# Performance work log

Measured on AMD Instinct MI355X. Metric: run time of the kernel, lower is better.

## Reference

```python
import jax, jax.numpy as jnp
import numpy as np

D_MODEL = 1024
NHEAD = 16
HEAD_DIM = D_MODEL // NHEAD
WINDOW = 64


def setup_inputs() -> dict:
    key = jax.random.key(0)
    ks = jax.random.split(key, 5)
    B, S = 1, 4096
    x = jax.random.normal(ks[0], (B, S, D_MODEL), dtype=jnp.float32)
    scale = 0.02
    Wq = jax.random.normal(ks[1], (D_MODEL, D_MODEL), dtype=jnp.float32) * scale
    Wk = jax.random.normal(ks[2], (D_MODEL, D_MODEL), dtype=jnp.float32) * scale
    Wv = jax.random.normal(ks[3], (D_MODEL, D_MODEL), dtype=jnp.float32) * scale
    Wo = jax.random.normal(ks[4], (D_MODEL, D_MODEL), dtype=jnp.float32) * scale
    return {"x": x, "Wq": Wq, "Wk": Wk, "Wv": Wv, "Wo": Wo}


def reference(x, Wq, Wk, Wv, Wo):
    B, S, D = x.shape
    H, hd, W = NHEAD, HEAD_DIM, WINDOW
    # projections (torch Linear: y = x @ W.T)
    q = (x @ Wq.T).reshape(B, S, H, hd).transpose(0, 2, 1, 3)  # [B,H,S,hd]
    k = (x @ Wk.T).reshape(B, S, H, hd).transpose(0, 2, 1, 3)
    v = (x @ Wv.T).reshape(B, S, H, hd).transpose(0, 2, 1, 3)
    # sliding window indices: each query attends to [i-W+1, i]
    qpos = jnp.arange(S)
    offsets = jnp.arange(-W + 1, 1)
    key_idx = qpos[:, None] + offsets[None, :]          # [S,W]
    valid = (key_idx >= 0) & (key_idx < S)
    key_idx = jnp.clip(key_idx, 0, S - 1)
    # gather windows: [B,H,S,W,hd]
    kw = jnp.take(k, key_idx, axis=2)
    vw = jnp.take(v, key_idx, axis=2)
    scores = jnp.einsum('bhsd,bhswd->bhsw', q, kw) / (hd ** 0.5)
    scores = jnp.where(valid[None, None, :, :], scores, -jnp.inf)
    attn = jax.nn.softmax(scores, axis=-1)
    out = jnp.einsum('bhsw,bhswd->bhsd', attn, vw)      # [B,H,S,hd]
    out = out.transpose(0, 2, 1, 3).reshape(B, S, D)
    return out @ Wo.T
```

## Files before the change

kernel.cpp:

```cpp
#include <hip/hip_runtime.h>
#include <cstdint>

typedef unsigned short u16;
using bf16x8 = __attribute__((ext_vector_type(8))) short;
using u16x8  = __attribute__((ext_vector_type(8))) unsigned short;
using f32x4  = __attribute__((ext_vector_type(4))) float;

#define DM 1024

__device__ __forceinline__ u16 f2b(float f) {
    union { float f; unsigned u; } v; v.f = f;
    unsigned r = v.u + 0x7FFFu + ((v.u >> 16) & 1u);
    return (u16)(r >> 16);
}
__device__ __forceinline__ float b2f(u16 b) {
    union { unsigned u; float f; } v; v.u = ((unsigned)b) << 16;
    return v.f;
}

#define GLL(gp, lp) __builtin_amdgcn_global_load_lds( \
    (const __attribute__((address_space(1))) void*)(uintptr_t)(gp), \
    (__attribute__((address_space(3))) void*)(unsigned)(uintptr_t)(lp), 16, 0, 0)

#define BAR()    __builtin_amdgcn_s_barrier()
#define WAITV4() asm volatile("s_waitcnt vmcnt(4)" ::: "memory")
#define WAITV0() asm volatile("s_waitcnt vmcnt(0)" ::: "memory")

__global__ __launch_bounds__(256) void cvt_all(const float* __restrict__ x,
                                               const float* __restrict__ Wq,
                                               const float* __restrict__ Wk,
                                               const float* __restrict__ Wv,
                                               const float* __restrict__ Wo,
                                               u16* __restrict__ xb,
                                               u16* __restrict__ wqkv,
                                               u16* __restrict__ wob) {
    size_t v = ((size_t)blockIdx.x * 256 + threadIdx.x) << 3;
    const float* src; u16* dst; size_t off;
    if (v < (size_t)4194304) { src = x; dst = xb; off = v; }
    else {
        size_t w = v - 4194304; int s = (int)(w >> 20); off = w & 1048575;
        src = (s == 0) ? Wq : (s == 1) ? Wk : (s == 2) ? Wv : Wo;
        dst = (s < 3) ? (wqkv + ((size_t)s << 20)) : wob;
    }
    const f32x4* p = (const f32x4*)(src + off);
    f32x4 a = p[0], b = p[1];
    u16x8 o;
    o[0] = f2b(a[0]); o[1] = f2b(a[1]); o[2] = f2b(a[2]); o[3] = f2b(a[3]);
    o[4] = f2b(b[0]); o[5] = f2b(b[1]); o[6] = f2b(b[2]); o[7] = f2b(b[3]);
    *(u16x8*)(dst + off) = o;
}

#define MROW(af_, bf_, d) \
    acc[d][0] = __builtin_amdgcn_mfma_f32_16x16x32_bf16(af_, bf_[0], acc[d][0], 0, 0, 0); \
    acc[d][1] = __builtin_amdgcn_mfma_f32_16x16x32_bf16(af_, bf_[1], acc[d][1], 0, 0, 0); \
    acc[d][2] = __builtin_amdgcn_mfma_f32_16x16x32_bf16(af_, bf_[2], acc[d][2], 0, 0, 0); \
    acc[d][3] = __builtin_amdgcn_mfma_f32_16x16x32_bf16(af_, bf_[3], acc[d][3], 0, 0, 0);

#define MFMA16(af_, bf_, ib) do { \
    __builtin_amdgcn_s_setprio(1); \
    MROW(af_[0], bf_, (ib) + 0) \
    MROW(af_[1], bf_, (ib) + 1) \
    MROW(af_[2], bf_, (ib) + 2) \
    MROW(af_[3], bf_, (ib) + 3) \
    __builtin_amdgcn_s_setprio(0); } while (0)

__global__ __launch_bounds__(512, 2) void gemm_qkv8(const u16* __restrict__ A,
                                                    const u16* __restrict__ B,
                                                    u16* __restrict__ Q,
                                                    u16* __restrict__ Ko,
                                                    u16* __restrict__ V) {
    __shared__ __align__(16) u16 As[2 * 16384];
    __shared__ __align__(16) u16 Bs[2 * 16384];
    const int tid  = threadIdx.x;
    const int lane = tid & 63;
    const int wid  = tid >> 6;
    const int wr   = wid >> 2;
    const int wc   = wid & 3;
    const int fr   = lane & 15;
    const int fg   = lane >> 4;
    const int brow = blockIdx.y << 8;
    const int bcol = blockIdx.x << 8;

    const int srow = tid >> 3;
    const int scol = ((tid & 7) ^ (srow & 7)) << 3;
    const u16* Ag = A + (size_t)(brow + srow) * 1024 + scol;
    const u16* Bg = B + (size_t)(bcol + srow) * 1024 + scol;

#define STG_A(buf, kt, c) GLL(Ag + (size_t)(c) * 65536 + (kt) * 64, \
                              (char*)As + (buf) * 32768 + (c) * 8192 + (wid << 10))
#define STG_B(buf, kt, c) GLL(Bg + (size_t)(c) * 65536 + (kt) * 64, \
                              (char*)Bs + (buf) * 32768 + (c) * 8192 + (wid << 10))

    const int swz  = (fr & 7) << 3;
    const int col0 = (fg << 3) ^ swz;
    const int col1 = (32 + (fg << 3)) ^ swz;
    const int aro  = ((wr << 7) + fr) << 6;
    const int bro  = ((wc << 6) + fr) << 6;

#define LDA4(dst, bufo, ih, cl) do { \
    const u16* p_ = As + (bufo) + aro + ((ih) << 12) + (cl); \
    dst[0] = *(const bf16x8*)(p_); \
    dst[1] = *(const bf16x8*)(p_ + 1024); \
    dst[2] = *(const bf16x8*)(p_ + 2048); \
    dst[3] = *(const bf16x8*)(p_ + 3072); } while (0)

#define LDB4(dst, bufo, cl) do { \
    const u16* p_ = Bs + (bufo) + bro + (cl); \
    dst[0] = *(const bf16x8*)(p_); \
    dst[1] = *(const bf16x8*)(p_ + 1024); \
    dst[2] = *(const bf16x8*)(p_ + 2048); \
    dst[3] = *(const bf16x8*)(p_ + 3072); } while (0)

    f32x4 acc[8][4];
    const f32x4 z = {0.f, 0.f, 0.f, 0.f};
    #pragma unroll
    for (int i = 0; i < 8; ++i)
        #pragma unroll
        for (int j = 0; j < 4; ++j) acc[i][j] = z;

    bf16x8 af0[4], af1[4], bf0[4], bf1[4];

    STG_B(0, 0, 0); STG_B(0, 0, 1); STG_B(0, 0, 2); STG_B(0, 0, 3);
    STG_A(0, 0, 0); STG_A(0, 0, 1); STG_A(0, 0, 2); STG_A(0, 0, 3);
    STG_B(1, 1, 0); STG_B(1, 1, 1); STG_B(1, 1, 2); STG_B(1, 1, 3);
    WAITV4();
    BAR();

    #pragma unroll 1
    for (int t = 0; t < 7; ++t) {
        const int k1 = 2 * t + 1, k2 = 2 * t + 2, k3 = 2 * t + 3;
        LDA4(af0, 0, 0, col0); LDB4(bf0, 0, col0);
        STG_A(1, k1, 0); STG_A(1, k1, 1);
        BAR(); MFMA16(af0, bf0, 0); BAR();
        LDA4(af1, 0, 0, col1); LDB4(bf1, 0, col1);
        STG_A(1, k1, 2); STG_A(1, k1, 3);
        BAR(); MFMA16(af1, bf1, 0); BAR();
        LDA4(af0, 0, 1, col0);
        STG_B(0, k2, 0); STG_B(0, k2, 1);
        BAR(); MFMA16(af0, bf0, 4); BAR();
        LDA4(af1, 0, 1, col1);
        STG_B(0, k2, 2); STG_B(0, k2, 3);
        BAR(); MFMA16(af1, bf1, 4); WAITV4(); BAR();
        LDA4(af0, 16384, 0, col0); LDB4(bf0, 16384, col0);
        STG_A(0, k2, 0); STG_A(0, k2, 1);
        BAR(); MFMA16(af0, bf0, 0); BAR();
        LDA4(af1, 16384, 0, col1); LDB4(bf1, 16384, col1);
        STG_A(0, k2, 2); STG_A(0, k2, 3);
        BAR(); MFMA16(af1, bf1, 0); BAR();
        LDA4(af0, 16384, 1, col0);
        STG_B(1, k3, 0); STG_B(1, k3, 1);
        BAR(); MFMA16(af0, bf0, 4); BAR();
        LDA4(af1, 16384, 1, col1);
        STG_B(1, k3, 2); STG_B(1, k3, 3);
        BAR(); MFMA16(af1, bf1, 4); WAITV4(); BAR();
    }
    LDA4(af0, 0, 0, col0); LDB4(bf0, 0, col0);
    STG_A(1, 15, 0); STG_A(1, 15, 1);
    BAR(); MFMA16(af0, bf0, 0); BAR();
    LDA4(af1, 0, 0, col1); LDB4(bf1, 0, col1);
    STG_A(1, 15, 2); STG_A(1, 15, 3);
    BAR(); MFMA16(af1, bf1, 0); BAR();
    LDA4(af0, 0, 1, col0);
    BAR(); MFMA16(af0, bf0, 4); BAR();
    LDA4(af1, 0, 1, col1);
    BAR(); MFMA16(af1, bf1, 4); WAITV0(); BAR();
    LDA4(af0, 16384, 0, col0); LDB4(bf0, 16384, col0);
    BAR(); MFMA16(af0, bf0, 0); BAR();
    LDA4(af1, 16384, 0, col1); LDB4(bf1, 16384, col1);
    BAR(); MFMA16(af1, bf1, 0); BAR();
    LDA4(af0, 16384, 1, col0);
    BAR(); MFMA16(af0, bf0, 4); BAR();
    LDA4(af1, 16384, 1, col1);
    BAR(); MFMA16(af1, bf1, 4);

    const int which = bcol >> 10;
    u16* O = (which == 0) ? Q : ((which == 1) ? Ko : V);
    const int ocol0 = (bcol & 1023) + (wc << 6);
    const int orow0 = brow + (wr << 7);
    #pragma unroll
    for (int i = 0; i < 8; ++i)
        #pragma unroll
        for (int j = 0; j < 4; ++j)
            #pragma unroll
            for (int r = 0; r < 4; ++r) {
                const int row = orow0 + i * 16 + fg * 4 + r;
                const int col = ocol0 + j * 16 + fr;
                O[(size_t)row * 1024 + col] = f2b(acc[i][j][r]);
            }
#undef STG_A
#undef STG_B
#undef LDA4
#undef LDB4
}

__device__ __forceinline__ void gemm_core_1024(const u16* __restrict__ A,
                                               const u16* __restrict__ B,
                                               int brow, int bcol,
                                               u16* Asb, u16* Bsb,
                                               f32x4 acc[4][4]) {
    const int tid  = threadIdx.x;
    const int lane = tid & 63;
    const int wid  = tid >> 6;
    const int wrow = (wid >> 1) << 6;
    const int wcol = (wid & 1) << 6;
    const int fr   = lane & 15;
    const int fk   = (lane >> 4) << 3;

    const size_t aBase = (size_t)(brow + (tid >> 2)) * 1024 + ((tid & 3) << 3);
    const size_t bBase = (size_t)(bcol + (tid >> 2)) * 1024 + ((tid & 3) << 3);
    const int wOff = wid << 10;

    const f32x4 z = {0.f, 0.f, 0.f, 0.f};
    #pragma unroll
    for (int i = 0; i < 4; ++i)
        #pragma unroll
        for (int j = 0; j < 4; ++j) acc[i][j] = z;

#define STAGE(bufi, kt) do { \
        const u16* ga_ = A + aBase + ((size_t)(kt) << 5); \
        const u16* gb_ = B + bBase + ((size_t)(kt) << 5); \
        char* la_ = (char*)(Asb + ((bufi) << 12)) + wOff; \
        char* lb_ = (char*)(Bsb + ((bufi) << 12)) + wOff; \
        GLL(ga_, la_); GLL(ga_ + (size_t)64 * 1024, la_ + 4096); \
        GLL(gb_, lb_); GLL(gb_ + (size_t)64 * 1024, lb_ + 4096); \
    } while (0)

    STAGE(0, 0);
    #pragma unroll 2
    for (int kt = 0; kt < 32; ++kt) {
        const int buf = kt & 1;
        __syncthreads();
        if (kt + 1 < 32) STAGE(buf ^ 1, kt + 1);
        const u16* As = Asb + (buf << 12);
        const u16* Bs = Bsb + (buf << 12);
        bf16x8 af[4], bfr[4];
        #pragma unroll
        for (int i = 0; i < 4; ++i)
            af[i] = *(const bf16x8*)(As + ((wrow + (i << 4) + fr) << 5) + fk);
        #pragma unroll
        for (int j = 0; j < 4; ++j)
            bfr[j] = *(const bf16x8*)(Bs + ((wcol + (j << 4) + fr) << 5) + fk);
        #pragma unroll
        for (int i = 0; i < 4; ++i)
            #pragma unroll
            for (int j = 0; j < 4; ++j)
                acc[i][j] = __builtin_amdgcn_mfma_f32_16x16x32_bf16(af[i], bfr[j], acc[i][j], 0, 0, 0);
    }
#undef STAGE
}

__global__ __launch_bounds__(256) void gemm_out(const u16* __restrict__ A,
                                                const u16* __restrict__ B,
                                                float* __restrict__ C) {
    __shared__ __align__(16) u16 As[2 * 128 * 32];
    __shared__ __align__(16) u16 Bs[2 * 128 * 32];
    const int brow = blockIdx.y << 7;
    const int bcol = blockIdx.x << 7;
    f32x4 acc[4][4];
    gemm_core_1024(A, B, brow, bcol, As, Bs, acc);

    const int lane = threadIdx.x & 63;
    const int wid  = threadIdx.x >> 6;
    const int wrow = (wid >> 1) << 6;
    const int wcol = (wid & 1) << 6;
    const int g = lane >> 4, c = lane & 15;
    #pragma unroll
    for (int i = 0; i < 4; ++i)
        #pragma unroll
        for (int j = 0; j < 4; ++j)
            #pragma unroll
            for (int r = 0; r < 4; ++r) {
                const int row = brow + wrow + i * 16 + g * 4 + r;
                const int col = bcol + wcol + j * 16 + c;
                C[(size_t)row * 1024 + col] = acc[i][j][r];
            }
}

__global__ __launch_bounds__(256) void attn_kernel(const u16* __restrict__ Qg,
                                                   const u16* __restrict__ Kg,
                                                   const u16* __restrict__ Vg,
                                                   u16* __restrict__ Og) {
    const int qb  = blockIdx.x;
    const int h   = blockIdx.y;
    const int tid = threadIdx.x;
    const int lane = tid & 63;
    const int w  = tid >> 6;
    const int fr = lane & 15;
    const int fg = lane >> 4;

    __shared__ __align__(16) u16 QK[64 * 72 + 128 * 72];
    __shared__ __align__(16) u16 Vt[64 * 136];
    __shared__ float Mrow[64][4];
    __shared__ float Lrow[64][4];

    u16* Qs = QK;
    u16* Ks = QK + 64 * 72;
    u16* Ps = QK;

    const int hoff  = h * 64;
    const int qrow0 = qb * 64;
    const int krow0 = qrow0 - 64;

    {
        const int r  = tid >> 3;
        const int c0 = (tid & 7) * 8;
        #pragma unroll
        for (int it = 0; it < 2; ++it) {
            const int row = r + it * 32;
            u16x8 val = *(const u16x8*)(Qg + (size_t)(qrow0 + row) * DM + hoff + c0);
            u16x8 o;
            #pragma unroll
            for (int e = 0; e < 8; ++e) o[e] = f2b(b2f(val[e]) * 0.125f);
            *(u16x8*)(Qs + row * 72 + c0) = o;
        }
        #pragma unroll
        for (int it = 0; it < 4; ++it) {
            const int row  = r + it * 32;
            const int grow = krow0 + row;
            u16x8 val = {0, 0, 0, 0, 0, 0, 0, 0};
            if (grow >= 0) val = *(const u16x8*)(Kg + (size_t)grow * DM + hoff + c0);
            *(u16x8*)(Ks + row * 72 + c0) = val;
        }
        #pragma unroll
        for (int it = 0; it < 4; ++it) {
            const int j    = r + it * 32;
            const int grow = krow0 + j;
            u16x8 val = {0, 0, 0, 0, 0, 0, 0, 0};
            if (grow >= 0) val = *(const u16x8*)(Vg + (size_t)grow * DM + hoff + c0);
            #pragma unroll
            for (int e = 0; e < 8; ++e) Vt[(c0 + e) * 136 + j] = val[e];
        }
    }
    __syncthreads();

    const f32x4 z = {0.f, 0.f, 0.f, 0.f};
    f32x4 s[4][2];
    #pragma unroll
    for (int i = 0; i < 4; ++i) { s[i][0] = z; s[i][1] = z; }
    #pragma unroll
    for (int kk = 0; kk < 2; ++kk) {
        const int k0 = kk * 32 + fg * 8;
        bf16x8 aq[4];
        #pragma unroll
        for (int i = 0; i < 4; ++i)
            aq[i] = *(const bf16x8*)(Qs + (i * 16 + fr) * 72 + k0);
        #pragma unroll
        for (int n = 0; n < 2; ++n) {
            const bf16x8 bk = *(const bf16x8*)(Ks + (w * 32 + n * 16 + fr) * 72 + k0);
            #pragma unroll
            for (int i = 0; i < 4; ++i)
                s[i][n] = __builtin_amdgcn_mfma_f32_16x16x32_bf16(aq[i], bk, s[i][n], 0, 0, 0);
        }
    }

    #pragma unroll
    for (int i = 0; i < 4; ++i) {
        #pragma unroll
        for (int r = 0; r < 4; ++r) {
            const int irow = i * 16 + fg * 4 + r;
            float mx = -3.0e38f;
            #pragma unroll
            for (int n = 0; n < 2; ++n) {
                const int jcol = w * 32 + n * 16 + fr;
                const bool valid = (jcol >= irow + 1) && (jcol <= irow + 64) && (krow0 + jcol >= 0);
                const float v = valid ? s[i][n][r] : -3.0e38f;
                s[i][n][r] = v;
                mx = fmaxf(mx, v);
            }
            #pragma unroll
            for (int d = 1; d < 16; d <<= 1) mx = fmaxf(mx, __shfl_xor(mx, d));
            if (fr == 0) Mrow[irow][w] = mx;
        }
    }
    __syncthreads();

    #pragma unroll
    for (int i = 0; i < 4; ++i) {
        #pragma unroll
        for (int r = 0; r < 4; ++r) {
            const int irow = i * 16 + fg * 4 + r;
            const float M = fmaxf(fmaxf(Mrow[irow][0], Mrow[irow][1]),
                                  fmaxf(Mrow[irow][2], Mrow[irow][3]));
            float sum = 0.f;
            #pragma unroll
            for (int n = 0; n < 2; ++n) {
                const float v = s[i][n][r];
                const float p = (v > -1.0e38f) ? __expf(v - M) : 0.f;
                sum += p;
                Ps[irow * 136 + (w * 32 + n * 16 + fr)] = f2b(p);
            }
            #pragma unroll
            for (int d = 1; d < 16; d <<= 1) sum += __shfl_xor(sum, d);
            if (fr == 0) Lrow[irow][w] = sum;
        }
    }
    __syncthreads();

    f32x4 o[4] = {z, z, z, z};
    #pragma unroll
    for (int ks = 0; ks < 4; ++ks) {
        const int k0 = ks * 32 + fg * 8;
        const bf16x8 ap = *(const bf16x8*)(Ps + (w * 16 + fr) * 136 + k0);
        #pragma unroll
        for (int n = 0; n < 4; ++n) {
            const bf16x8 bv = *(const bf16x8*)(Vt + (n * 16 + fr) * 136 + k0);
            o[n] = __builtin_amdgcn_mfma_f32_16x16x32_bf16(ap, bv, o[n], 0, 0, 0);
        }
    }

    #pragma unroll
    for (int r = 0; r < 4; ++r) {
        const int irow = w * 16 + fg * 4 + r;
        const float L = Lrow[irow][0] + Lrow[irow][1] + Lrow[irow][2] + Lrow[irow][3];
        const float rl = 1.0f / L;
        #pragma unroll
        for (int n = 0; n < 4; ++n)
            Og[(size_t)(qrow0 + irow) * DM + hoff + n * 16 + fr] = f2b(o[n][r] * rl);
    }
}

extern "C" void kernel_launch(void* const* d_in, const int* in_sizes, int n_in,
                              void* d_out, int out_size, void* d_ws, size_t ws_size,
                              hipStream_t stream) {
    (void)in_sizes; (void)n_in; (void)out_size; (void)ws_size;
    const float* x  = (const float*)d_in[0];
    const float* Wq = (const float*)d_in[1];
    const float* Wk = (const float*)d_in[2];
    const float* Wv = (const float*)d_in[3];
    const float* Wo = (const float*)d_in[4];
    float* out = (float*)d_out;

    char* ws = (char*)d_ws;
    u16* xb   = (u16*)(ws);
    u16* Wqkv = (u16*)(ws + ((size_t)8  << 20));
    u16* Wob  = (u16*)(ws + ((size_t)14 << 20));
    u16* qb   = (u16*)(ws + ((size_t)16 << 20));
    u16* kb   = (u16*)(ws + ((size_t)24 << 20));
    u16* vb   = (u16*)(ws + ((size_t)32 << 20));
    u16* ab   = (u16*)(ws + ((size_t)40 << 20));

    cvt_all<<<4096, 256, 0, stream>>>(x, Wq, Wk, Wv, Wo, xb, Wqkv, Wob);
    gemm_qkv8<<<dim3(12, 16), 512, 0, stream>>>(xb, Wqkv, qb, kb, vb);
    attn_kernel<<<dim3(64, 16), 256, 0, stream>>>(qb, kb, vb, ab);
    gemm_out<<<dim3(8, 32), 256, 0, stream>>>(ab, Wob, out);
}
```

Baseline: 88.81 us.

## Retile QKV GEMM to 256x192 blocks filling all CUs with interleaved QKV output

Changes the QKV projection tile from 256x256 to 256x192 so the grid becomes 256 blocks, matching the CU count instead of leaving a partial wave. Block indices are remapped with an XCD-style swizzle, and Q/K/V are written into one interleaved buffer with a 3072 stride that attention reads directly. The attention V-transpose LDS stride is padded to reduce bank conflicts. Smaller B tiles lower per-block reuse and change the load/wait accounting.

```diff
diff --git a/kernel.cpp b/kernel.cpp
--- a/kernel.cpp
+++ b/kernel.cpp
@@ -23,7 +23,7 @@
     (__attribute__((address_space(3))) void*)(unsigned)(uintptr_t)(lp), 16, 0, 0)
 
 #define BAR()    __builtin_amdgcn_s_barrier()
-#define WAITV4() asm volatile("s_waitcnt vmcnt(4)" ::: "memory")
+#define WAITV3() asm volatile("s_waitcnt vmcnt(3)" ::: "memory")
 #define WAITV0() asm volatile("s_waitcnt vmcnt(0)" ::: "memory")
 
 __global__ __launch_bounds__(256) void cvt_all(const float* __restrict__ x,
@@ -50,27 +50,24 @@
     *(u16x8*)(dst + off) = o;
 }
 
-#define MROW(af_, bf_, d) \
+#define MROW3(af_, bf_, d) \
     acc[d][0] = __builtin_amdgcn_mfma_f32_16x16x32_bf16(af_, bf_[0], acc[d][0], 0, 0, 0); \
     acc[d][1] = __builtin_amdgcn_mfma_f32_16x16x32_bf16(af_, bf_[1], acc[d][1], 0, 0, 0); \
-    acc[d][2] = __builtin_amdgcn_mfma_f32_16x16x32_bf16(af_, bf_[2], acc[d][2], 0, 0, 0); \
-    acc[d][3] = __builtin_amdgcn_mfma_f32_16x16x32_bf16(af_, bf_[3], acc[d][3], 0, 0, 0);
-
-#define MFMA16(af_, bf_, ib) do { \
+    acc[d][2] = __builtin_amdgcn_mfma_f32_16x16x32_bf16(af_, bf_[2], acc[d][2], 0, 0, 0);
+
+#define MFMA12(af_, bf_, ib) do { \
     __builtin_amdgcn_s_setprio(1); \
-    MROW(af_[0], bf_, (ib) + 0) \
-    MROW(af_[1], bf_, (ib) + 1) \
-    MROW(af_[2], bf_, (ib) + 2) \
-    MROW(af_[3], bf_, (ib) + 3) \
+    MROW3(af_[0], bf_, (ib) + 0) \
+    MROW3(af_[1], bf_, (ib) + 1) \
+    MROW3(af_[2], bf_, (ib) + 2) \
+    MROW3(af_[3], bf_, (ib) + 3) \
     __builtin_amdgcn_s_setprio(0); } while (0)
 
 __global__ __launch_bounds__(512, 2) void gemm_qkv8(const u16* __restrict__ A,
                                                     const u16* __restrict__ B,
-                                                    u16* __restrict__ Q,
-                                                    u16* __restrict__ Ko,
-                                                    u16* __restrict__ V) {
+                                                    u16* __restrict__ QKV) {
     __shared__ __align__(16) u16 As[2 * 16384];
-    __shared__ __align__(16) u16 Bs[2 * 16384];
+    __shared__ __align__(16) u16 Bs[2 * 12288];
     const int tid  = threadIdx.x;
     const int lane = tid & 63;
     const int wid  = tid >> 6;
@@ -78,8 +75,11 @@
     const int wc   = wid & 3;
     const int fr   = lane & 15;
     const int fg   = lane >> 4;
-    const int brow = blockIdx.y << 8;
-    const int bcol = blockIdx.x << 8;
+
+    const int hw   = blockIdx.y * 16 + blockIdx.x;
+    const int lg   = (hw & 7) * 32 + (hw >> 3);
+    const int brow = (lg >> 4) << 8;
+    const int bcol = (lg & 15) * 192;
 
     const int srow = tid >> 3;
     const int scol = ((tid & 7) ^ (srow & 7)) << 3;
@@ -89,13 +89,13 @@
 #define STG_A(buf, kt, c) GLL(Ag + (size_t)(c) * 65536 + (kt) * 64, \
                               (char*)As + (buf) * 32768 + (c) * 8192 + (wid << 10))
 #define STG_B(buf, kt, c) GLL(Bg + (size_t)(c) * 65536 + (kt) * 64, \
-                              (char*)Bs + (buf) * 32768 + (c) * 8192 + (wid << 10))
+                              (char*)Bs + (buf) * 24576 + (c) * 8192 + (wid << 10))
 
     const int swz  = (fr & 7) << 3;
     const int col0 = (fg << 3) ^ swz;
     const int col1 = (32 + (fg << 3)) ^ swz;
     const int aro  = ((wr << 7) + fr) << 6;
-    const int bro  = ((wc << 6) + fr) << 6;
+    const int bro  = ((wc * 48) + fr) << 6;
 
 #define LDA4(dst, bufo, ih, cl) do { \
     const u16* p_ = As + (bufo) + aro + ((ih) << 12) + (cl); \
@@ -104,93 +104,90 @@
     dst[2] = *(const bf16x8*)(p_ + 2048); \
     dst[3] = *(const bf16x8*)(p_ + 3072); } while (0)
 
-#define LDB4(dst, bufo, cl) do { \
+#define LDB3(dst, bufo, cl) do { \
     const u16* p_ = Bs + (bufo) + bro + (cl); \
     dst[0] = *(const bf16x8*)(p_); \
     dst[1] = *(const bf16x8*)(p_ + 1024); \
-    dst[2] = *(const bf16x8*)(p_ + 2048); \
-    dst[3] = *(const bf16x8*)(p_ + 3072); } while (0)
-
-    f32x4 acc[8][4];
+    dst[2] = *(const bf16x8*)(p_ + 2048); } while (0)
+
+    f32x4 acc[8][3];
     const f32x4 z = {0.f, 0.f, 0.f, 0.f};
     #pragma unroll
     for (int i = 0; i < 8; ++i)
         #pragma unroll
-        for (int j = 0; j < 4; ++j) acc[i][j] = z;
-
-    bf16x8 af0[4], af1[4], bf0[4], bf1[4];
-
-    STG_B(0, 0, 0); STG_B(0, 0, 1); STG_B(0, 0, 2); STG_B(0, 0, 3);
+        for (int j = 0; j < 3; ++j) acc[i][j] = z;
+
+    bf16x8 af0[4], af1[4], bf0[3], bf1[3];
+
+    STG_B(0, 0, 0); STG_B(0, 0, 1); STG_B(0, 0, 2);
     STG_A(0, 0, 0); STG_A(0, 0, 1); STG_A(0, 0, 2); STG_A(0, 0, 3);
-    STG_B(1, 1, 0); STG_B(1, 1, 1); STG_B(1, 1, 2); STG_B(1, 1, 3);
-    WAITV4();
+    STG_B(1, 1, 0); STG_B(1, 1, 1); STG_B(1, 1, 2);
+    WAITV3();
     BAR();
 
     #pragma unroll 1
     for (int t = 0; t < 7; ++t) {
         const int k1 = 2 * t + 1, k2 = 2 * t + 2, k3 = 2 * t + 3;
-        LDA4(af0, 0, 0, col0); LDB4(bf0, 0, col0);
+        LDA4(af0, 0, 0, col0); LDB3(bf0, 0, col0);
         STG_A(1, k1, 0); STG_A(1, k1, 1);
-        BAR(); MFMA16(af0, bf0, 0); BAR();
-        LDA4(af1, 0, 0, col1); LDB4(bf1, 0, col1);
+        BAR(); MFMA12(af0, bf0, 0); BAR();
+        LDA4(af1, 0, 0, col1); LDB3(bf1, 0, col1);
         STG_A(1, k1, 2); STG_A(1, k1, 3);
-        BAR(); MFMA16(af1, bf1, 0); BAR();
+        BAR(); MFMA12(af1, bf1, 0); BAR();
         LDA4(af0, 0, 1, col0);
         STG_B(0, k2, 0); STG_B(0, k2, 1);
-        BAR(); MFMA16(af0, bf0, 4); BAR();
+        BAR(); MFMA12(af0, bf0, 4); BAR();
         LDA4(af1, 0, 1, col1);
-        STG_B(0, k2, 2); STG_B(0, k2, 3);
-        BAR(); MFMA16(af1, bf1, 4); WAITV4(); BAR();
-        LDA4(af0, 16384, 0, col0); LDB4(bf0, 16384, col0);
+        STG_B(0, k2, 2);
+        BAR(); MFMA12(af1, bf1, 4); WAITV3(); BAR();
+        LDA4(af0, 16384, 0, col0); LDB3(bf0, 12288, col0);
         STG_A(0, k2, 0); STG_A(0, k2, 1);
-        BAR(); MFMA16(af0, bf0, 0); BAR();
-        LDA4(af1, 16384, 0, col1); LDB4(bf1, 16384, col1);
+        BAR(); MFMA12(af0, bf0, 0); BAR();
+        LDA4(af1, 16384, 0, col1); LDB3(bf1, 12288, col1);
         STG_A(0, k2, 2); STG_A(0, k2, 3);
-        BAR(); MFMA16(af1, bf1, 0); BAR();
+        BAR(); MFMA12(af1, bf1, 0); BAR();
         LDA4(af0, 16384, 1, col0);
         STG_B(1, k3, 0); STG_B(1, k3, 1);
-        BAR(); MFMA16(af0, bf0, 4); BAR();
+        BAR(); MFMA12(af0, bf0, 4); BAR();
         LDA4(af1, 16384, 1, col1);
-        STG_B(1, k3, 2); STG_B(1, k3, 3);
-        BAR(); MFMA16(af1, bf1, 4); WAITV4(); BAR();
-    }
-    LDA4(af0, 0, 0, col0); LDB4(bf0, 0, col0);
+        STG_B(1, k3, 2);
+        BAR(); MFMA12(af1, bf1, 4); WAITV3(); BAR();
+    }
+    LDA4(af0, 0, 0, col0); LDB3(bf0, 0, col0);
     STG_A(1, 15, 0); STG_A(1, 15, 1);
-    BAR(); MFMA16(af0, bf0, 0); BAR();
-    LDA4(af1, 0, 0, col1); LDB4(bf1, 0, col1);
+    BAR(); MFMA12(af0, bf0, 0); BAR();
+    LDA4(af1, 0, 0, col1); LDB3(bf1, 0, col1);
     STG_A(1, 15, 2); STG_A(1, 15, 3);
-    BAR(); MFMA16(af1, bf1, 0); BAR();
+    BAR(); MFMA12(af1, bf1, 0); BAR();
     LDA4(af0, 0, 1, col0);
-    BAR(); MFMA16(af0, bf0, 4); BAR();
+    BAR(); MFMA12(af0, bf0, 4); BAR();
     LDA4(af1, 0, 1, col1);
-    BAR(); MFMA16(af1, bf1, 4); WAITV0(); BAR();
-    LDA4(af0, 16384, 0, col0); LDB4(bf0, 16384, col0);
-    BAR(); MFMA16(af0, bf0, 0); BAR();
-    LDA4(af1, 16384, 0, col1); LDB4(bf1, 16384, col1);
-    BAR(); MFMA16(af1, bf1, 0); BAR();
+    BAR(); MFMA12(af1, bf1, 4); WAITV0(); BAR();
+    LDA4(af0, 16384, 0, col0); LDB3(bf0, 12288, col0);
+    BAR(); MFMA12(af0, bf0, 0); BAR();
+    LDA4(af1, 16384, 0, col1); LDB3(bf1, 12288, col1);
+    BAR(); MFMA12(af1, bf1, 0); BAR();
     LDA4(af0, 16384, 1, col0);
-    BAR(); MFMA16(af0, bf0, 4); BAR();
+    BAR(); MFMA12(af0, bf0, 4); BAR();
     LDA4(af1, 16384, 1, col1);
-    BAR(); MFMA16(af1, bf1, 4);
-
-    const int which = bcol >> 10;
-    u16* O = (which == 0) ? Q : ((which == 1) ? Ko : V);
-    const int ocol0 = (bcol & 1023) + (wc << 6);
+    BAR(); MFMA12(af1, bf1, 4);
+
+    const int ocol0 = bcol + wc * 48;
     const int orow0 = brow + (wr << 7);
     #pragma unroll
     for (int i = 0; i < 8; ++i)
         #pragma unroll
-        for (int j = 0; j < 4; ++j)
+        for (int j = 0; j < 3; ++j)
             #pragma unroll
             for (int r = 0; r < 4; ++r) {
                 const int row = orow0 + i * 16 + fg * 4 + r;
                 const int col = ocol0 + j * 16 + fr;
-                O[(size_t)row * 1024 + col] = f2b(acc[i][j][r]);
+                QKV[(size_t)row * 3072 + col] = f2b(acc[i][j][r]);
             }
 #undef STG_A
 #undef STG_B
 #undef LDA4
-#undef LDB4
+#undef LDB3
 }
 
 __device__ __forceinline__ void gemm_core_1024(const u16* __restrict__ A,
@@ -276,9 +273,7 @@
             }
 }
 
-__global__ __launch_bounds__(256) void attn_kernel(const u16* __restrict__ Qg,
-                                                   const u16* __restrict__ Kg,
-                                                   const u16* __restrict__ Vg,
+__global__ __launch_bounds__(256) void attn_kernel(const u16* __restrict__ QKV,
                                                    u16* __restrict__ Og) {
     const int qb  = blockIdx.x;
     const int h   = blockIdx.y;
@@ -289,7 +284,7 @@
     const int fg = lane >> 4;
 
     __shared__ __align__(16) u16 QK[64 * 72 + 128 * 72];
-    __shared__ __align__(16) u16 Vt[64 * 136];
+    __shared__ __align__(16) u16 Vt[64 * 138];
     __shared__ float Mrow[64][4];
     __shared__ float Lrow[64][4];
 
@@ -297,6 +292,10 @@
     u16* Ks = QK + 64 * 72;
     u16* Ps = QK;
 
+    const u16* Qg = QKV;
+    const u16* Kg = QKV + 1024;
+    const u16* Vg = QKV + 2048;
+
     const int hoff  = h * 64;
     const int qrow0 = qb * 64;
     const int krow0 = qrow0 - 64;
@@ -307,7 +306,7 @@
         #pragma unroll
         for (int it = 0; it < 2; ++it) {
             const int row = r + it * 32;
-            u16x8 val = *(const u16x8*)(Qg + (size_t)(qrow0 + row) * DM + hoff + c0);
+            u16x8 val = *(const u16x8*)(Qg + (size_t)(qrow0 + row) * 3072 + hoff + c0);
             u16x8 o;
             #pragma unroll
             for (int e = 0; e < 8; ++e) o[e] = f2b(b2f(val[e]) * 0.125f);
@@ -318,7 +317,7 @@
             const int row  = r + it * 32;
             const int grow = krow0 + row;
             u16x8 val = {0, 0, 0, 0, 0, 0, 0, 0};
-            if (grow >= 0) val = *(const u16x8*)(Kg + (size_t)grow * DM + hoff + c0);
+            if (grow >= 0) val = *(const u16x8*)(Kg + (size_t)grow * 3072 + hoff + c0);
             *(u16x8*)(Ks + row * 72 + c0) = val;
         }
         #pragma unroll
@@ -326,9 +325,9 @@
             const int j    = r + it * 32;
             const int grow = krow0 + j;
             u16x8 val = {0, 0, 0, 0, 0, 0, 0, 0};
-            if (grow >= 0) val = *(const u16x8*)(Vg + (size_t)grow * DM + hoff + c0);
-            #pragma unroll
-            for (int e = 0; e < 8; ++e) Vt[(c0 + e) * 136 + j] = val[e];
+            if (grow >= 0) val = *(const u16x8*)(Vg + (size_t)grow * 3072 + hoff + c0);
+            #pragma unroll
+            for (int e = 0; e < 8; ++e) Vt[(c0 + e) * 138 + j] = val[e];
         }
     }
     __syncthreads();
@@ -403,7 +402,7 @@
         const bf16x8 ap = *(const bf16x8*)(Ps + (w * 16 + fr) * 136 + k0);
         #pragma unroll
         for (int n = 0; n < 4; ++n) {
-            const bf16x8 bv = *(const bf16x8*)(Vt + (n * 16 + fr) * 136 + k0);
+            const bf16x8 bv = *(const bf16x8*)(Vt + (n * 16 + fr) * 138 + k0);
             o[n] = __builtin_amdgcn_mfma_f32_16x16x32_bf16(ap, bv, o[n], 0, 0, 0);
         }
     }
@@ -434,13 +433,11 @@
     u16* xb   = (u16*)(ws);
     u16* Wqkv = (u16*)(ws + ((size_t)8  << 20));
     u16* Wob  = (u16*)(ws + ((size_t)14 << 20));
-    u16* qb   = (u16*)(ws + ((size_t)16 << 20));
-    u16* kb   = (u16*)(ws + ((size_t)24 << 20));
-    u16* vb   = (u16*)(ws + ((size_t)32 << 20));
+    u16* qkvb = (u16*)(ws + ((size_t)16 << 20));
     u16* ab   = (u16*)(ws + ((size_t)40 << 20));
 
     cvt_all<<<4096, 256, 0, stream>>>(x, Wq, Wk, Wv, Wo, xb, Wqkv, Wob);
-    gemm_qkv8<<<dim3(12, 16), 512, 0, stream>>>(xb, Wqkv, qb, kb, vb);
-    attn_kernel<<<dim3(64, 16), 256, 0, stream>>>(qb, kb, vb, ab);
+    gemm_qkv8<<<dim3(16, 16), 512, 0, stream>>>(xb, Wqkv, qkvb);
+    attn_kernel<<<dim3(64, 16), 256, 0, stream>>>(qkvb, ab);
     gemm_out<<<dim3(8, 32), 256, 0, stream>>>(ab, Wob, out);
 }
```

Result: faster. 85.67 us (-3.5%).
